# Kernel tuning notes

Measured on AMD Instinct MI355X. Metric: run time of the kernel, lower is better.

The kernel has to match this reference:

```python
import jax, jax.numpy as jnp
import numpy as np

VOCAB, EMB, HID = 32000, 256, 512
B, S = 16, 256


def setup_inputs() -> dict:
    key = jax.random.key(0)
    ks = jax.random.split(key, 7)
    x = jax.random.randint(ks[0], (B, S), 0, VOCAB, dtype=jnp.int32)
    E = jax.random.normal(ks[1], (VOCAB, EMB), dtype=jnp.float32) * 0.02
    # GRUCell kernels, gate order [z, r, h], reset_after=True (keras default)
    W = jax.random.normal(ks[2], (EMB, 3 * HID), dtype=jnp.float32) * 0.02
    U = jax.random.normal(ks[3], (HID, 3 * HID), dtype=jnp.float32) * 0.02
    b = jnp.zeros((2, 3 * HID), dtype=jnp.float32)  # [input_bias, recurrent_bias]
    Wd = jax.random.normal(ks[4], (HID, VOCAB), dtype=jnp.float32) * 0.02
    bd = jnp.zeros((VOCAB,), dtype=jnp.float32)
    return {"x": x, "E": E, "W": W, "U": U, "b": b, "Wd": Wd, "bd": bd}


def _gru_sequence(emb, W, U, b):
    # emb: [B, S, EMB]. Precompute all input-side gate projections at once.
    xw = jnp.einsum('bse,eh->bsh', emb, W) + b[0]          # [B, S, 3H]
    xw_t = jnp.transpose(xw, (1, 0, 2))                     # [S, B, 3H]
    b_rec = b[1]
    H = U.shape[0]

    def step(h, xt):
        rec = h @ U + b_rec                                 # [B, 3H]
        xz, xr, xh = xt[:, :H], xt[:, H:2 * H], xt[:, 2 * H:]
        rz, rr, rh = rec[:, :H], rec[:, H:2 * H], rec[:, 2 * H:]
        z = jax.nn.sigmoid(xz + rz)
        r = jax.nn.sigmoid(xr + rr)
        hh = jnp.tanh(xh + r * rh)                          # reset_after=True form
        h_new = z * h + (1.0 - z) * hh
        return h_new, h_new

    h0 = jnp.zeros((emb.shape[0], H), dtype=emb.dtype)
    _, hs = jax.lax.scan(step, h0, xw_t)                    # hs: [S, B, H]
    return jnp.transpose(hs, (1, 0, 2))                     # [B, S, H]


def reference(x, E, W, U, b, Wd, bd):
    emb = E[x]                                              # [B, S, EMB]
    h = _gru_sequence(emb, W, U, b)                         # [B, S, H]
    logits = jnp.einsum('bsh,hv->bsv', h, Wd) + bd          # [B, S, VOCAB]
    return logits
```

## Files before the change

kernel.cpp:

```cpp
#include <hip/hip_runtime.h>
#include <hip/hip_bf16.h>
#include <stdint.h>
#include <stddef.h>

#define NB 16
#define NS 256
#define NH 512
#define NE 256
#define NV 32000
#define NM (NB*NS)
#define N3H 1536

typedef __attribute__((ext_vector_type(8))) short short8v;
typedef __attribute__((ext_vector_type(4))) float float4v;
typedef __attribute__((address_space(1))) const unsigned int gas_u32;
typedef __attribute__((address_space(3))) unsigned int las_u32;

static __device__ __forceinline__ unsigned short f2bf(float f) {
  __hip_bfloat16 h = __float2bfloat16(f);
  return *reinterpret_cast<unsigned short*>(&h);
}
static __device__ __forceinline__ float bf2f(unsigned short u) {
  union { unsigned int u; float f; } c;
  c.u = ((unsigned int)u) << 16;
  return c.f;
}
static __device__ __forceinline__ float fast_tanh(float x) {
  float t = __expf(2.f * x);
  return (t - 1.f) / (t + 1.f);
}

__global__ void gather_emb(const int* __restrict__ x, const float* __restrict__ E,
                           unsigned short* __restrict__ A) {
  int m = blockIdx.x * 4 + (threadIdx.x >> 6);
  int lane = threadIdx.x & 63;
  int t = x[m];
  float4 v = reinterpret_cast<const float4*>(E + (size_t)t * NE)[lane];
  ushort4 o = make_ushort4(f2bf(v.x), f2bf(v.y), f2bf(v.z), f2bf(v.w));
  reinterpret_cast<ushort4*>(A + (size_t)m * NE)[lane] = o;
}

template<typename T>
__global__ void transpose_conv(const float* __restrict__ in, T* __restrict__ out,
                               int R, int C) {
  __shared__ float tile[32][33];
  int c0 = blockIdx.x * 32, r0 = blockIdx.y * 32;
  int tx = threadIdx.x, ty = threadIdx.y;
  #pragma unroll
  for (int i = 0; i < 32; i += 8)
    tile[ty + i][tx] = in[(size_t)(r0 + ty + i) * C + (c0 + tx)];
  __syncthreads();
  #pragma unroll
  for (int i = 0; i < 32; i += 8) {
    float v = tile[tx][ty + i];
    if constexpr (sizeof(T) == 2)
      out[(size_t)(c0 + ty + i) * R + (r0 + tx)] = (T)f2bf(v);
    else
      out[(size_t)(c0 + ty + i) * R + (r0 + tx)] = (T)v;
  }
}

template<bool OUT_BF16>
__launch_bounds__(256)
__global__ void gemm_bt(const unsigned short* __restrict__ A,
                        const unsigned short* __restrict__ BT,
                        const float* __restrict__ bias,
                        void* __restrict__ out, int N, int K) {
  __shared__ unsigned short As[128 * 32];
  __shared__ unsigned short Bs[128 * 32];
  const int tid = threadIdx.x;
  const int lane = tid & 63, wave = tid >> 6;
  const int wr = wave >> 1, wc = wave & 1;
  int nwg = gridDim.x * gridDim.y;
  int bid0 = blockIdx.y * gridDim.x + blockIdx.x;
  int q = nwg >> 3, r8 = nwg & 7;
  int xcd = bid0 & 7, idx = bid0 >> 3;
  int bid = (xcd < r8 ? xcd * (q + 1) : r8 * (q + 1) + (xcd - r8) * q) + idx;
  const int m0 = (bid / gridDim.x) * 128, n0 = (bid % gridDim.x) * 128;
  const int lr = lane & 15, lg = lane >> 4;
  float4v acc[4][4] = {};

  for (int k0 = 0; k0 < K; k0 += 32) {
    #pragma unroll
    for (int qq = 0; qq < 2; ++qq) {
      int byteoff = qq * 4096 + tid * 16;
      int rr = byteoff >> 6, cb = byteoff & 63;
      const char* ga = (const char*)A + ((size_t)(m0 + rr) * K + k0) * 2 + cb;
      const char* gb = (const char*)BT + ((size_t)(n0 + rr) * K + k0) * 2 + cb;
      char* la = (char*)As + qq * 4096 + wave * 1024;
      char* lb = (char*)Bs + qq * 4096 + wave * 1024;
      __builtin_amdgcn_global_load_lds((gas_u32*)ga, (las_u32*)la, 16, 0, 0);
      __builtin_amdgcn_global_load_lds((gas_u32*)gb, (las_u32*)lb, 16, 0, 0);
    }
    __syncthreads();
    short8v a[4], b[4];
    #pragma unroll
    for (int i = 0; i < 4; ++i)
      a[i] = *(const short8v*)((const char*)As + (wr * 64 + i * 16 + lr) * 64 + lg * 16);
    #pragma unroll
    for (int j = 0; j < 4; ++j)
      b[j] = *(const short8v*)((const char*)Bs + (wc * 64 + j * 16 + lr) * 64 + lg * 16);
    #pragma unroll
    for (int i = 0; i < 4; ++i) {
      #pragma unroll
      for (int j = 0; j < 4; ++j)
        acc[i][j] = __builtin_amdgcn_mfma_f32_16x16x32_bf16(a[i], b[j], acc[i][j], 0, 0, 0);
    }
    __syncthreads();
  }
  #pragma unroll
  for (int i = 0; i < 4; ++i) {
    int row = m0 + wr * 64 + i * 16 + lg * 4;
    #pragma unroll
    for (int j = 0; j < 4; ++j) {
      int col = n0 + wc * 64 + j * 16 + lr;
      float bv = bias[col];
      #pragma unroll
      for (int rr = 0; rr < 4; ++rr) {
        float v = acc[i][j][rr] + bv;
        if constexpr (OUT_BF16)
          ((unsigned short*)out)[(size_t)(row + rr) * N + col] = f2bf(v);
        else
          ((float*)out)[(size_t)(row + rr) * N + col] = v;
      }
    }
  }
}

#define SENT 0xFFFFFFFFu
__launch_bounds__(256, 1)
__global__ void gru_kernel(const unsigned short* __restrict__ xw,
                           const float* __restrict__ UT,
                           const float* __restrict__ bvec,
                           unsigned int* __restrict__ Hex) {
  const int blk = blockIdx.x, tid = threadIdx.x;
  const int grp = blk >> 3, wq = blk & 7;
  const int lane = tid & 63, w = tid >> 6;
  const int lg = lane >> 4, lr = lane & 15;
  __shared__ __align__(16) unsigned short h_lds[2][1024];
  __shared__ __align__(16) float scratch[4][96];

  const int D0w = 64 * wq + 16 * w;
  short8v Bf[3][16];
  #pragma unroll
  for (int c = 0; c < 3; ++c) {
    const float* up = UT + (size_t)(c * 512 + D0w + lr) * 512 + lg * 8;
    #pragma unroll
    for (int kk = 0; kk < 16; ++kk) {
      float4 v0 = *(const float4*)(up + kk * 32);
      float4 v1 = *(const float4*)(up + kk * 32 + 4);
      short8v t;
      t[0] = (short)f2bf(v0.x); t[1] = (short)f2bf(v0.y);
      t[2] = (short)f2bf(v0.z); t[3] = (short)f2bf(v0.w);
      t[4] = (short)f2bf(v1.x); t[5] = (short)f2bf(v1.y);
      t[6] = (short)f2bf(v1.z); t[7] = (short)f2bf(v1.w);
      Bf[c][kk] = t;
    }
  }
  reinterpret_cast<uint4*>(h_lds)[tid] = make_uint4(0, 0, 0, 0);

  const int b = lane & 1, di = lane >> 1;
  const int d = D0w + di, hi = d & 1;
  float h_old = 0.f, bz = 0.f, br = 0.f, bh = 0.f;
  const unsigned int* xp = nullptr;
  if (lane < 32) {
    const float* brec = bvec + 1536;
    bz = brec[d]; br = brec[512 + d]; bh = brec[1024 + d];
    xp = (const unsigned int*)xw + (size_t)(grp * 2 + b) * 256 * 768 + (d >> 1);
  }
  const bool own = ((tid >> 4) & 7) == wq;
  const int pbb = tid >> 7;
  const int pm  = (2 * tid) & 255;
  __syncthreads();

  int p = 0;
  for (int s = 0; s < 256; ++s) {
    unsigned int xzw = 0, xrw = 0, xhw = 0;
    if (lane < 32) { xzw = xp[0]; xrw = xp[256]; xhw = xp[512]; xp += 768; }

    if (s > 0 && !own) {
      const unsigned long long* src =
          (const unsigned long long*)(Hex + (size_t)s * 4096 + grp * 512 + 2 * tid);
      unsigned long long v = __hip_atomic_load(src, __ATOMIC_RELAXED, __HIP_MEMORY_SCOPE_AGENT);
      while ((unsigned int)v == SENT || (unsigned int)(v >> 32) == SENT) {
        __builtin_amdgcn_s_sleep(1);
        v = __hip_atomic_load(src, __ATOMIC_RELAXED, __HIP_MEMORY_SCOPE_AGENT);
      }
      *(unsigned long long*)((char*)h_lds[p] + ((pbb * 1024 + pm * 4) ^ (pbb << 4))) = v;
    }
    __syncthreads();

    float4v a0 = {}, a1 = {}, a2 = {};
    const char* hb = (const char*)h_lds[p];
    #pragma unroll
    for (int kk = 0; kk < 16; ++kk) {
      int off = ((lane & 1) * 1024 + kk * 64 + lg * 16) ^ ((lane & 1) << 4);
      short8v a = *(const short8v*)(hb + off);
      a0 = __builtin_amdgcn_mfma_f32_16x16x32_bf16(a, Bf[0][kk], a0, 0, 0, 0);
      a1 = __builtin_amdgcn_mfma_f32_16x16x32_bf16(a, Bf[1][kk], a1, 0, 0, 0);
      a2 = __builtin_amdgcn_mfma_f32_16x16x32_bf16(a, Bf[2][kk], a2, 0, 0, 0);
    }
    if (lg == 0) {
      *(float2*)&scratch[w][lr * 2]      = make_float2(a0[0], a0[1]);
      *(float2*)&scratch[w][32 + lr * 2] = make_float2(a1[0], a1[1]);
      *(float2*)&scratch[w][64 + lr * 2] = make_float2(a2[0], a2[1]);
    }
    if (lane < 32) {
      float rz = scratch[w][di * 2 + b];
      float rr = scratch[w][32 + di * 2 + b];
      float rh = scratch[w][64 + di * 2 + b];
      float xz = bf2f((unsigned short)(hi ? (xzw >> 16) : (xzw & 0xffff)));
      float xr = bf2f((unsigned short)(hi ? (xrw >> 16) : (xrw & 0xffff)));
      float xh = bf2f((unsigned short)(hi ? (xhw >> 16) : (xhw & 0xffff)));
      float z = 1.f / (1.f + __expf(-(xz + rz + bz)));
      float r = 1.f / (1.f + __expf(-(xr + rr + br)));
      float hh = fast_tanh(xh + r * (rh + bh));
      h_old = z * h_old + (1.f - z) * hh;
      unsigned int mine = f2bf(h_old);
      unsigned int pack = mine | ((unsigned int)__shfl_xor((int)mine, 2) << 16);
      unsigned int hip2 = (unsigned int)__shfl_xor((int)pack, 4);
      if ((lane & 6) == 0) {
        unsigned long long u = (unsigned long long)pack | ((unsigned long long)hip2 << 32);
        int m = 32 * wq + 8 * w + 2 * (lane >> 3);
        __hip_atomic_store((unsigned long long*)&Hex[(size_t)(s + 1) * 4096 + grp * 512 +
                                                     b * 256 + m],
                           u, __ATOMIC_RELAXED, __HIP_MEMORY_SCOPE_AGENT);
        *(unsigned long long*)((char*)h_lds[p ^ 1] + ((b * 1024 + m * 4) ^ (b << 4))) = u;
      }
    }
    p ^= 1;
  }
}

__launch_bounds__(256)
__global__ void dec_gemm(const char* __restrict__ HexB,
                         const unsigned short* __restrict__ WdT,
                         const float* __restrict__ bd,
                         float* __restrict__ out) {
  __shared__ unsigned short As[128 * 32];
  __shared__ unsigned short Bs[128 * 32];
  const int tid = threadIdx.x;
  const int lane = tid & 63, wave = tid >> 6;
  const int wr = wave >> 1, wc = wave & 1;
  const int lr = lane & 15, lg = lane >> 4;
  int bid0 = blockIdx.x;
  int bid = (bid0 & 7) * 1000 + (bid0 >> 3);
  const int mt = bid & 31, nt = bid >> 5;
  const int b = mt >> 1, s0 = (mt & 1) * 128;
  const int n0 = nt * 128;
  float4v acc[4][4] = {};

  for (int k0 = 0; k0 < NH; k0 += 32) {
    #pragma unroll
    for (int qq = 0; qq < 2; ++qq) {
      int off = qq * 4096 + tid * 16;
      int rloc = off >> 6, cb = off & 63;
      int s = s0 + rloc;
      const char* ga = HexB + ((size_t)(s + 1) * 4096 + (b >> 1) * 512 + (b & 1) * 256) * 4
                       + k0 * 2 + cb;
      const char* gb = (const char*)WdT + ((size_t)(n0 + rloc) * 512 + k0) * 2 + cb;
      __builtin_amdgcn_global_load_lds((gas_u32*)ga,
          (las_u32*)((char*)As + qq * 4096 + wave * 1024), 16, 0, 0);
      __builtin_amdgcn_global_load_lds((gas_u32*)gb,
          (las_u32*)((char*)Bs + qq * 4096 + wave * 1024), 16, 0, 0);
    }
    __syncthreads();
    short8v a[4], bb[4];
    #pragma unroll
    for (int i = 0; i < 4; ++i)
      a[i] = *(const short8v*)((const char*)As + (wr * 64 + i * 16 + lr) * 64 + lg * 16);
    #pragma unroll
    for (int j = 0; j < 4; ++j)
      bb[j] = *(const short8v*)((const char*)Bs + (wc * 64 + j * 16 + lr) * 64 + lg * 16);
    #pragma unroll
    for (int i = 0; i < 4; ++i) {
      #pragma unroll
      for (int j = 0; j < 4; ++j)
        acc[i][j] = __builtin_amdgcn_mfma_f32_16x16x32_bf16(a[i], bb[j], acc[i][j], 0, 0, 0);
    }
    __syncthreads();
  }
  #pragma unroll
  for (int i = 0; i < 4; ++i) {
    int l = wr * 64 + i * 16 + lg * 4;
    #pragma unroll
    for (int j = 0; j < 4; ++j) {
      int col = n0 + wc * 64 + j * 16 + lr;
      float bv = bd[col];
      #pragma unroll
      for (int rr = 0; rr < 4; ++rr) {
        size_t m = (size_t)(b * 256 + s0 + l + rr);
        __builtin_nontemporal_store(acc[i][j][rr] + bv, &out[m * NV + col]);
      }
    }
  }
}

extern "C" void kernel_launch(void* const* d_in, const int* in_sizes, int n_in,
                              void* d_out, int out_size, void* d_ws, size_t ws_size,
                              hipStream_t stream) {
  const int*   x  = (const int*)d_in[0];
  const float* E  = (const float*)d_in[1];
  const float* W  = (const float*)d_in[2];
  const float* U  = (const float*)d_in[3];
  const float* bv = (const float*)d_in[4];
  const float* Wd = (const float*)d_in[5];
  const float* bd = (const float*)d_in[6];
  float* out = (float*)d_out;

  char* ws = (char*)d_ws;
  size_t off = 0;
  auto alloc = [&](size_t bytes) -> void* {
    void* p = ws + off;
    off = (off + bytes + 255) & ~(size_t)255;
    return p;
  };
  unsigned short* Aemb = (unsigned short*)alloc((size_t)NM * NE * 2);
  unsigned short* WT   = (unsigned short*)alloc((size_t)N3H * NE * 2);
  float*          UT   = (float*)alloc((size_t)N3H * NH * 4);
  unsigned short* xwb  = (unsigned short*)alloc((size_t)NM * N3H * 2);
  unsigned short* WdT  = (unsigned short*)alloc((size_t)NV * NH * 2);
  unsigned int*   Hex  = (unsigned int*)alloc((size_t)257 * 4096 * 4);

  hipMemsetAsync(Hex, 0xFF, (size_t)257 * 4096 * 4, stream);

  gather_emb<<<NM / 4, 256, 0, stream>>>(x, E, Aemb);
  transpose_conv<unsigned short><<<dim3(N3H / 32, NE / 32), dim3(32, 8), 0, stream>>>(W,  WT,  NE, N3H);
  transpose_conv<float>         <<<dim3(N3H / 32, NH / 32), dim3(32, 8), 0, stream>>>(U,  UT,  NH, N3H);
  transpose_conv<unsigned short><<<dim3(NV / 32,  NH / 32), dim3(32, 8), 0, stream>>>(Wd, WdT, NH, NV);

  gemm_bt<true><<<dim3(N3H / 128, NM / 128), 256, 0, stream>>>(Aemb, WT, bv, xwb, N3H, NE);

  gru_kernel<<<64, 256, 0, stream>>>(xwb, UT, bv, Hex);

  dec_gemm<<<8000, 256, 0, stream>>>((const char*)Hex, WdT, bd, out);
}
```

Baseline: 672.2 us.

## Process four batch groups per GRU block, shrinking grid from 64 to 16

Each GRU block now handles four independent batch-pair groups in an unrolled inner loop, keeping separate LDS hidden buffers and h state per group. The grid drops from 64 to 16 blocks, so U weights are loaded into registers by fewer blocks. Work on one group can overlap another group's cross-block spin-wait on the exchange buffer. In exchange, each block does four times the serial work per timestep and adds a __syncthreads per group, which may lengthen the critical path.

After: 1.859 ms. +176.6%, slower.

```diff
diff --git a/kernel.cpp b/kernel.cpp
--- a/kernel.cpp
+++ b/kernel.cpp
@@ -134,10 +134,10 @@
                            const float* __restrict__ bvec,
                            unsigned int* __restrict__ Hex) {
   const int blk = blockIdx.x, tid = threadIdx.x;
-  const int grp = blk >> 3, wq = blk & 7;
+  const int quad = blk >> 3, wq = blk & 7;
   const int lane = tid & 63, w = tid >> 6;
   const int lg = lane >> 4, lr = lane & 15;
-  __shared__ __align__(16) unsigned short h_lds[2][1024];
+  __shared__ __align__(16) unsigned short h_lds[4][2][1024];
   __shared__ __align__(16) float scratch[4][96];
 
   const int D0w = 64 * wq + 16 * w;
@@ -157,16 +157,21 @@
       Bf[c][kk] = t;
     }
   }
-  reinterpret_cast<uint4*>(h_lds)[tid] = make_uint4(0, 0, 0, 0);
+  for (int i = tid; i < 1024; i += 256)
+    reinterpret_cast<uint4*>(h_lds)[i] = make_uint4(0, 0, 0, 0);
 
   const int b = lane & 1, di = lane >> 1;
   const int d = D0w + di, hi = d & 1;
-  float h_old = 0.f, bz = 0.f, br = 0.f, bh = 0.f;
-  const unsigned int* xp = nullptr;
+  float h_old[4] = {0.f, 0.f, 0.f, 0.f};
+  float bz = 0.f, br = 0.f, bh = 0.f;
+  const unsigned int* xp[4] = {nullptr, nullptr, nullptr, nullptr};
   if (lane < 32) {
     const float* brec = bvec + 1536;
     bz = brec[d]; br = brec[512 + d]; bh = brec[1024 + d];
-    xp = (const unsigned int*)xw + (size_t)(grp * 2 + b) * 256 * 768 + (d >> 1);
+    #pragma unroll
+    for (int c = 0; c < 4; ++c)
+      xp[c] = (const unsigned int*)xw +
+              (size_t)((quad * 4 + c) * 2 + b) * 256 * 768 + (d >> 1);
   }
   const bool own = ((tid >> 4) & 7) == wq;
   const int pbb = tid >> 7;
@@ -175,57 +180,62 @@
 
   int p = 0;
   for (int s = 0; s < 256; ++s) {
-    unsigned int xzw = 0, xrw = 0, xhw = 0;
-    if (lane < 32) { xzw = xp[0]; xrw = xp[256]; xhw = xp[512]; xp += 768; }
-
-    if (s > 0 && !own) {
-      const unsigned long long* src =
-          (const unsigned long long*)(Hex + (size_t)s * 4096 + grp * 512 + 2 * tid);
-      unsigned long long v = __hip_atomic_load(src, __ATOMIC_RELAXED, __HIP_MEMORY_SCOPE_AGENT);
-      while ((unsigned int)v == SENT || (unsigned int)(v >> 32) == SENT) {
-        __builtin_amdgcn_s_sleep(1);
-        v = __hip_atomic_load(src, __ATOMIC_RELAXED, __HIP_MEMORY_SCOPE_AGENT);
-      }
-      *(unsigned long long*)((char*)h_lds[p] + ((pbb * 1024 + pm * 4) ^ (pbb << 4))) = v;
-    }
-    __syncthreads();
-
-    float4v a0 = {}, a1 = {}, a2 = {};
-    const char* hb = (const char*)h_lds[p];
-    #pragma unroll
-    for (int kk = 0; kk < 16; ++kk) {
-      int off = ((lane & 1) * 1024 + kk * 64 + lg * 16) ^ ((lane & 1) << 4);
-      short8v a = *(const short8v*)(hb + off);
-      a0 = __builtin_amdgcn_mfma_f32_16x16x32_bf16(a, Bf[0][kk], a0, 0, 0, 0);
-      a1 = __builtin_amdgcn_mfma_f32_16x16x32_bf16(a, Bf[1][kk], a1, 0, 0, 0);
-      a2 = __builtin_amdgcn_mfma_f32_16x16x32_bf16(a, Bf[2][kk], a2, 0, 0, 0);
-    }
-    if (lg == 0) {
-      *(float2*)&scratch[w][lr * 2]      = make_float2(a0[0], a0[1]);
-      *(float2*)&scratch[w][32 + lr * 2] = make_float2(a1[0], a1[1]);
-      *(float2*)&scratch[w][64 + lr * 2] = make_float2(a2[0], a2[1]);
-    }
-    if (lane < 32) {
-      float rz = scratch[w][di * 2 + b];
-      float rr = scratch[w][32 + di * 2 + b];
-      float rh = scratch[w][64 + di * 2 + b];
-      float xz = bf2f((unsigned short)(hi ? (xzw >> 16) : (xzw & 0xffff)));
-      float xr = bf2f((unsigned short)(hi ? (xrw >> 16) : (xrw & 0xffff)));
-      float xh = bf2f((unsigned short)(hi ? (xhw >> 16) : (xhw & 0xffff)));
-      float z = 1.f / (1.f + __expf(-(xz + rz + bz)));
-      float r = 1.f / (1.f + __expf(-(xr + rr + br)));
-      float hh = fast_tanh(xh + r * (rh + bh));
-      h_old = z * h_old + (1.f - z) * hh;
-      unsigned int mine = f2bf(h_old);
-      unsigned int pack = mine | ((unsigned int)__shfl_xor((int)mine, 2) << 16);
-      unsigned int hip2 = (unsigned int)__shfl_xor((int)pack, 4);
-      if ((lane & 6) == 0) {
-        unsigned long long u = (unsigned long long)pack | ((unsigned long long)hip2 << 32);
-        int m = 32 * wq + 8 * w + 2 * (lane >> 3);
-        __hip_atomic_store((unsigned long long*)&Hex[(size_t)(s + 1) * 4096 + grp * 512 +
-                                                     b * 256 + m],
-                           u, __ATOMIC_RELAXED, __HIP_MEMORY_SCOPE_AGENT);
-        *(unsigned long long*)((char*)h_lds[p ^ 1] + ((b * 1024 + m * 4) ^ (b << 4))) = u;
+    #pragma unroll
+    for (int c = 0; c < 4; ++c) {
+      const int grp = quad * 4 + c;
+      unsigned int xzw = 0, xrw = 0, xhw = 0;
+      if (lane < 32) {
+        xzw = xp[c][0]; xrw = xp[c][256]; xhw = xp[c][512]; xp[c] += 768;
+      }
+      if (s > 0 && !own) {
+        const unsigned long long* src =
+            (const unsigned long long*)(Hex + (size_t)s * 4096 + grp * 512 + 2 * tid);
+        unsigned long long v = __hip_atomic_load(src, __ATOMIC_RELAXED, __HIP_MEMORY_SCOPE_AGENT);
+        while ((unsigned int)v == SENT || (unsigned int)(v >> 32) == SENT) {
+          __builtin_amdgcn_s_sleep(1);
+          v = __hip_atomic_load(src, __ATOMIC_RELAXED, __HIP_MEMORY_SCOPE_AGENT);
+        }
+        *(unsigned long long*)((char*)h_lds[c][p] + ((pbb * 1024 + pm * 4) ^ (pbb << 4))) = v;
+      }
+      __syncthreads();
+
+      float4v a0 = {}, a1 = {}, a2 = {};
+      const char* hb = (const char*)h_lds[c][p];
+      #pragma unroll
+      for (int kk = 0; kk < 16; ++kk) {
+        int off = ((lane & 1) * 1024 + kk * 64 + lg * 16) ^ ((lane & 1) << 4);
+        short8v a = *(const short8v*)(hb + off);
+        a0 = __builtin_amdgcn_mfma_f32_16x16x32_bf16(a, Bf[0][kk], a0, 0, 0, 0);
+        a1 = __builtin_amdgcn_mfma_f32_16x16x32_bf16(a, Bf[1][kk], a1, 0, 0, 0);
+        a2 = __builtin_amdgcn_mfma_f32_16x16x32_bf16(a, Bf[2][kk], a2, 0, 0, 0);
+      }
+      if (lg == 0) {
+        *(float2*)&scratch[w][lr * 2]      = make_float2(a0[0], a0[1]);
+        *(float2*)&scratch[w][32 + lr * 2] = make_float2(a1[0], a1[1]);
+        *(float2*)&scratch[w][64 + lr * 2] = make_float2(a2[0], a2[1]);
+      }
+      if (lane < 32) {
+        float rz = scratch[w][di * 2 + b];
+        float rr = scratch[w][32 + di * 2 + b];
+        float rh = scratch[w][64 + di * 2 + b];
+        float xz = bf2f((unsigned short)(hi ? (xzw >> 16) : (xzw & 0xffff)));
+        float xr = bf2f((unsigned short)(hi ? (xrw >> 16) : (xrw & 0xffff)));
+        float xh = bf2f((unsigned short)(hi ? (xhw >> 16) : (xhw & 0xffff)));
+        float z = 1.f / (1.f + __expf(-(xz + rz + bz)));
+        float r = 1.f / (1.f + __expf(-(xr + rr + br)));
+        float hh = fast_tanh(xh + r * (rh + bh));
+        h_old[c] = z * h_old[c] + (1.f - z) * hh;
+        unsigned int mine = f2bf(h_old[c]);
+        unsigned int pack = mine | ((unsigned int)__shfl_xor((int)mine, 2) << 16);
+        unsigned int hip2 = (unsigned int)__shfl_xor((int)pack, 4);
+        if ((lane & 6) == 0) {
+          unsigned long long u = (unsigned long long)pack | ((unsigned long long)hip2 << 32);
+          int m = 32 * wq + 8 * w + 2 * (lane >> 3);
+          __hip_atomic_store((unsigned long long*)&Hex[(size_t)(s + 1) * 4096 + grp * 512 +
+                                                       b * 256 + m],
+                             u, __ATOMIC_RELAXED, __HIP_MEMORY_SCOPE_AGENT);
+          *(unsigned long long*)((char*)h_lds[c][p ^ 1] + ((b * 1024 + m * 4) ^ (b << 4))) = u;
+        }
       }
     }
     p ^= 1;
@@ -331,7 +341,7 @@
 
   gemm_bt<true><<<dim3(N3H / 128, NM / 128), 256, 0, stream>>>(Aemb, WT, bv, xwb, N3H, NE);
 
-  gru_kernel<<<64, 256, 0, stream>>>(xwb, UT, bv, Hex);
+  gru_kernel<<<16, 256, 0, stream>>>(xwb, UT, bv, Hex);
 
   dec_gemm<<<8000, 256, 0, stream>>>((const char*)Hex, WdT, bd, out);
 }
```
